# Kernel optimization log

Measured on AMD Instinct MI355X. Metric: run time of the kernel, lower is better.

## Reference

```python
import jax, jax.numpy as jnp
import numpy as np

C = 64  # channels fixed by module

def conv1x1(x, W, b):
    # x: [B,C,H,W], W: [C_out,C_in], b: [C_out]
    return jnp.einsum('bchw,oc->bohw', x, W) + b[None, :, None, None]

def setup_inputs() -> dict:
    key = jax.random.key(0)
    ks = jax.random.split(key, 16)
    B, H, W = 4, 64, 64
    inp = {
        'x_latter': jax.random.normal(ks[0], (B, C, H, W), jnp.float32),
        'x': jax.random.normal(ks[1], (B, C, H, W), jnp.float32),
    }
    scale = 1.0 / np.sqrt(C)
    names = ['high', 'low', 'value', 'e_conv', 'mid', 'latter']
    for i, n in enumerate(names):
        inp[f'W_{n}'] = jax.random.normal(ks[2 + 2 * i], (C, C), jnp.float32) * scale
        inp[f'b_{n}'] = jax.random.normal(ks[3 + 2 * i], (C,), jnp.float32) * 0.01
    return inp

def reference(x_latter, x, W_high, b_high, W_low, b_low, W_value, b_value,
              W_e_conv, b_e_conv, W_mid, b_mid, W_latter, b_latter):
    b, c, h, w = x_latter.shape
    hw = h * w
    # stage 1: channel-normalized spatial attention
    xl_hi = conv1x1(x_latter, W_high, b_high).reshape(b, c, hw)          # [b,c,hw]
    x_low = conv1x1(x, W_low, b_low).reshape(b, c, hw).transpose(0, 2, 1)  # [b,hw,c]
    p = jnp.einsum('bnc,bcm->bnm', x_low, xl_hi)                          # [b,hw,hw]
    p = jax.nn.softmax(p, axis=1)  # torch Softmax(dim=1) over first hw axis
    v = conv1x1(x, W_value, b_value).reshape(b, c, hw).transpose(0, 2, 1)  # [b,hw,c]
    e = jnp.einsum('bnm,bmc->bnc', p, v) + x_low                          # [b,hw,c]
    e = e.transpose(0, 2, 1).reshape(b, c, h, w)                          # [b,c,h,w]
    e = conv1x1(e, W_e_conv, b_e_conv).reshape(b, c, hw)                  # [b,c,hw]
    # stage 2: channel-channel attention
    xl2 = conv1x1(x_latter, W_latter, b_latter).reshape(b, c, hw).transpose(0, 2, 1)  # [b,hw,c]
    t = jnp.einsum('bcn,bnd->bcd', e, xl2)                                # [b,c,c]
    t = jax.nn.softmax(t, axis=1)
    x_mid = conv1x1(x, W_mid, b_mid).reshape(b, c, hw).transpose(0, 2, 1)  # [b,hw,c]
    out = jnp.einsum('bnc,bcd->bnd', x_mid, t)                            # [b,hw,c]
    return out.transpose(0, 2, 1).reshape(b, c, h, w)
```

## Files before the change

### kernel.cpp

```cpp
#include <hip/hip_runtime.h>
#include <math.h>

#define BATCH 4
#define CH 64
#define HW 4096

typedef __attribute__((ext_vector_type(8))) short short8;
typedef __attribute__((ext_vector_type(4))) float f32x4;
typedef __attribute__((ext_vector_type(4))) float float4v;

#define MFMA(a, b, c) __builtin_amdgcn_mfma_f32_16x16x32_bf16(a, b, c, 0, 0, 0)

__device__ __forceinline__ short f2bf(float f) {
    unsigned u = __builtin_bit_cast(unsigned, f);
    u += 0x7fffu + ((u >> 16) & 1u);
    return (short)(u >> 16);
}
__device__ __forceinline__ float bf2f(short s) {
    unsigned u = ((unsigned)(unsigned short)s) << 16;
    return __builtin_bit_cast(float, u);
}
__device__ __forceinline__ void gld16(const short* g, short* l) {
    __builtin_amdgcn_global_load_lds(
        (const __attribute__((address_space(1))) unsigned int*)g,
        (__attribute__((address_space(3))) unsigned int*)l, 16, 0, 0);
}

__global__ __launch_bounds__(256) void splitX(
    const float* __restrict__ x, const float* __restrict__ xl,
    short* __restrict__ XFh, short* __restrict__ XFl)
{
    int src = blockIdx.z, b = blockIdx.y, bx = blockIdx.x;
    const float* X = src ? xl : x;
    int t = threadIdx.x, wv = t >> 6, ln = t & 63;
    int nt = bx * 4 + wv;
    int n = (nt << 4) + (ln & 15);
    int g = ln >> 4;
    size_t sb = ((size_t)(src * BATCH + b) * 256 + nt) * 2;
    #pragma unroll
    for (int kt = 0; kt < 2; kt++) {
        short8 h, l;
        #pragma unroll
        for (int j = 0; j < 8; j++) {
            float v = X[(size_t)(b * 64 + kt * 32 + g * 8 + j) * HW + n];
            short hh = f2bf(v);
            h[j] = hh;
            l[j] = f2bf(v - bf2f(hh));
        }
        *(short8*)(XFh + (sb + kt) * 512 + (size_t)ln * 8) = h;
        *(short8*)(XFl + (sb + kt) * 512 + (size_t)ln * 8) = l;
    }
}

__global__ __launch_bounds__(256) void convm(
    const short* __restrict__ XFh, const short* __restrict__ XFl,
    const float* __restrict__ Wlow, const float* __restrict__ blow,
    const float* __restrict__ Wval, const float* __restrict__ bval,
    const float* __restrict__ Wmid, const float* __restrict__ bmid,
    const float* __restrict__ Wlat, const float* __restrict__ blat,
    const float* __restrict__ Whigh, const float* __restrict__ bhigh,
    float* __restrict__ XLOW, float* __restrict__ XMID, float* __restrict__ XL2,
    short* __restrict__ PAh, short* __restrict__ PAl,
    short* __restrict__ PBh, short* __restrict__ PBl,
    short* __restrict__ PVh, short* __restrict__ PVl)
{
    int mode = blockIdx.z, b = blockIdx.y, bx = blockIdx.x;
    const float* W; const float* bias; int src;
    switch (mode) {
        case 0:  W = Wlow;  bias = blow;  src = 0; break;
        case 1:  W = Wval;  bias = bval;  src = 0; break;
        case 2:  W = Wmid;  bias = bmid;  src = 0; break;
        case 3:  W = Wlat;  bias = blat;  src = 1; break;
        default: W = Whigh; bias = bhigh; src = 1; break;
    }
    int t = threadIdx.x, wv = t >> 6, ln = t & 63;
    int row = ln & 15, g = ln >> 4;

    short8 Wh[4][2], Wlo[4][2];
    #pragma unroll
    for (int ot = 0; ot < 4; ot++)
        #pragma unroll
        for (int kt = 0; kt < 2; kt++) {
            const float* wp = W + (ot * 16 + row) * 64 + kt * 32 + g * 8;
            short8 h, l;
            #pragma unroll
            for (int j = 0; j < 8; j++) {
                float v = wp[j];
                short hh = f2bf(v);
                h[j] = hh;
                l[j] = f2bf(v - bf2f(hh));
            }
            Wh[ot][kt] = h; Wlo[ot][kt] = l;
        }

    int nt = bx * 4 + wv;
    size_t xb = ((size_t)(src * BATCH + b) * 256 + nt) * 2;
    short8 Bh[2], Bl[2];
    #pragma unroll
    for (int kt = 0; kt < 2; kt++) {
        Bh[kt] = *(const short8*)(XFh + (xb + kt) * 512 + (size_t)ln * 8);
        Bl[kt] = *(const short8*)(XFl + (xb + kt) * 512 + (size_t)ln * 8);
    }

    f32x4 acc[4];
    #pragma unroll
    for (int ot = 0; ot < 4; ot++) {
        #pragma unroll
        for (int r = 0; r < 4; r++) acc[ot][r] = bias[ot * 16 + g * 4 + r];
    }
    #pragma unroll
    for (int ot = 0; ot < 4; ot++)
        #pragma unroll
        for (int kt = 0; kt < 2; kt++) {
            acc[ot] = MFMA(Wh[ot][kt], Bh[kt], acc[ot]);
            acc[ot] = MFMA(Wh[ot][kt], Bl[kt], acc[ot]);
            acc[ot] = MFMA(Wlo[ot][kt], Bh[kt], acc[ot]);
        }

    __shared__ float Ld[64][65];
    #pragma unroll
    for (int ot = 0; ot < 4; ot++)
        #pragma unroll
        for (int r = 0; r < 4; r++)
            Ld[wv * 16 + (ln & 15)][ot * 16 + g * 4 + r] = acc[ot][r];
    __syncthreads();

    int n0 = bx * 64;
    if (mode == 0 || mode == 2 || mode == 3) {
        float* outp = (mode == 0) ? XLOW : (mode == 2) ? XMID : XL2;
        int n = t >> 2, o0 = (t & 3) * 16;
        float vout[16];
        #pragma unroll
        for (int k = 0; k < 16; k++) vout[k] = Ld[n][o0 + k];
        float* gp = outp + ((size_t)b * HW + n0 + n) * 64 + o0;
        #pragma unroll
        for (int k = 0; k < 4; k++)
            *(float4v*)(gp + k * 4) = *(float4v*)(vout + k * 4);
    }
    if (mode == 0 || mode == 4) {
        short* Ph = (mode == 0) ? PAh : PBh;
        short* Pl = (mode == 0) ? PAl : PBl;
        #pragma unroll
        for (int kt = 0; kt < 2; kt++) {
            short8 h, l;
            #pragma unroll
            for (int j = 0; j < 8; j++) {
                float v = Ld[wv * 16 + (ln & 15)][kt * 32 + g * 8 + j];
                short hh = f2bf(v);
                h[j] = hh;
                l[j] = f2bf(v - bf2f(hh));
            }
            size_t blob = (((size_t)b * 256 + bx * 4 + wv) * 2 + kt) * 512 + (size_t)ln * 8;
            *(short8*)(Ph + blob) = h;
            *(short8*)(Pl + blob) = l;
        }
    }
    if (mode == 1) {
        int ktm_l = wv >> 1;
        int ct0 = (wv & 1) * 2;
        #pragma unroll
        for (int cc = 0; cc < 2; cc++) {
            int ct = ct0 + cc;
            int c = ct * 16 + (ln & 15);
            short8 h, l;
            #pragma unroll
            for (int j = 0; j < 8; j++) {
                float v = Ld[(ktm_l * 2 + (j >> 2)) * 16 + g * 4 + (j & 3)][c];
                short hh = f2bf(v);
                h[j] = hh;
                l[j] = f2bf(v - bf2f(hh));
            }
            size_t blob = (((size_t)b * 128 + bx * 2 + ktm_l) * 4 + ct) * 512 + (size_t)ln * 8;
            *(short8*)(PVh + blob) = h;
            *(short8*)(PVl + blob) = l;
        }
    }
}

__global__ __launch_bounds__(256) void zpass2(
    const short* __restrict__ PAh, const short* __restrict__ PAl,
    const short* __restrict__ PBh, const short* __restrict__ PBl,
    float* __restrict__ Zp)
{
    int bid = blockIdx.x;
    int sw = (bid & 7) * 128 + (bid >> 3);
    int mchunk = sw & 63, nc = (sw >> 6) & 3, b = sw >> 8;
    int t = threadIdx.x, wv = t >> 6, ln = t & 63;
    short8 bh[4][2], bl[4][2];
    #pragma unroll
    for (int msub = 0; msub < 4; msub++)
        #pragma unroll
        for (int kt = 0; kt < 2; kt++) {
            size_t o = ((size_t)(b * 256 + mchunk * 4 + msub) * 2 + kt) * 512 + ln * 8;
            bh[msub][kt] = *(const short8*)(PBh + o);
            bl[msub][kt] = *(const short8*)(PBl + o);
        }
    float zacc[4] = {0.f, 0.f, 0.f, 0.f};
    for (int s = 0; s < 16; s++) {
        int nt = nc * 64 + s * 4 + wv;
        size_t ab = ((size_t)(b * 256 + nt) * 2) * 512 + ln * 8;
        short8 ah0 = *(const short8*)(PAh + ab);
        short8 ah1 = *(const short8*)(PAh + ab + 512);
        short8 al0 = *(const short8*)(PAl + ab);
        short8 al1 = *(const short8*)(PAl + ab + 512);
        #pragma unroll
        for (int msub = 0; msub < 4; msub++) {
            f32x4 acc = {0.f, 0.f, 0.f, 0.f};
            acc = MFMA(ah0, bh[msub][0], acc);
            acc = MFMA(ah1, bh[msub][1], acc);
            acc = MFMA(ah0, bl[msub][0], acc);
            acc = MFMA(ah1, bl[msub][1], acc);
            acc = MFMA(al0, bh[msub][0], acc);
            acc = MFMA(al1, bh[msub][1], acc);
            zacc[msub] += __expf(acc[0]) + __expf(acc[1]) + __expf(acc[2]) + __expf(acc[3]);
        }
    }
    #pragma unroll
    for (int msub = 0; msub < 4; msub++) {
        zacc[msub] += __shfl_xor(zacc[msub], 16, 64);
        zacc[msub] += __shfl_xor(zacc[msub], 32, 64);
    }
    __shared__ float sZ[4][64];
    if (ln < 16) {
        #pragma unroll
        for (int msub = 0; msub < 4; msub++) sZ[wv][msub * 16 + ln] = zacc[msub];
    }
    __syncthreads();
    if (t < 64) {
        float z = sZ[0][t] + sZ[1][t] + sZ[2][t] + sZ[3][t];
        Zp[((size_t)(b * 4 + nc)) * 4096 + mchunk * 64 + t] = z;
    }
}

__global__ __launch_bounds__(256, 3) void epass8(
    const short* __restrict__ PAh, const short* __restrict__ PAl,
    const short* __restrict__ PBh, const short* __restrict__ PBl,
    const short* __restrict__ PVh, const short* __restrict__ PVl,
    const float* __restrict__ Zp, float* __restrict__ Ep, int nseg)
{
    int nwg = 32 * nseg * 4, cpx = nwg >> 3;
    int bid = blockIdx.x;
    int sw = (bid & 7) * cpx + (bid >> 3);
    int nb = sw & 31, mseg = (sw >> 5) % nseg, b = sw / (32 * nseg);
    int iters = 128 / nseg;
    int mper = 4096 / nseg;
    int t = threadIdx.x, wv = t >> 6, ln = t & 63;
    int lnm = ln & 15, lnr = ln >> 4;

    __shared__ __align__(16) short sB[2][2][2048];
    __shared__ __align__(16) short sV[2][2][2048];
    __shared__ __align__(16) float sZi[1024];

    for (int k = t; k < mper; k += 256) {
        int m = mseg * mper + k;
        float z = Zp[((size_t)(b * 4 + 0)) * 4096 + m]
                + Zp[((size_t)(b * 4 + 1)) * 4096 + m]
                + Zp[((size_t)(b * 4 + 2)) * 4096 + m]
                + Zp[((size_t)(b * 4 + 3)) * 4096 + m];
        sZi[k] = 1.f / z;
    }

    short8 Lh[2][2], Ll[2][2];
    #pragma unroll
    for (int rt = 0; rt < 2; rt++)
        #pragma unroll
        for (int kt = 0; kt < 2; kt++) {
            int nt = nb * 8 + wv * 2 + rt;
            size_t base = ((size_t)(b * 256 + nt) * 2 + kt) * 512 + ln * 8;
            Lh[rt][kt] = *(const short8*)(PAh + base);
            Ll[rt][kt] = *(const short8*)(PAl + base);
        }

    f32x4 acc_e[2][4];
    #pragma unroll
    for (int rt = 0; rt < 2; rt++)
        #pragma unroll
        for (int ct = 0; ct < 4; ct++) acc_e[rt][ct] = (f32x4){0.f, 0.f, 0.f, 0.f};

    const int mt00 = mseg * (mper >> 4);
    const int ktm0 = mseg * (mper >> 5);
    #define STAGE(bufi, ii) { \
        size_t pbb = (size_t)b * 262144 + (size_t)(mt00 + (ii) * 2) * 1024; \
        size_t pvb = (size_t)b * 262144 + (size_t)(ktm0 + (ii)) * 2048; \
        gld16(PBh + pbb + t * 8, &sB[bufi][0][wv * 512]); \
        gld16(PBl + pbb + t * 8, &sB[bufi][1][wv * 512]); \
        gld16(PVh + pvb + t * 8, &sV[bufi][0][wv * 512]); \
        gld16(PVl + pvb + t * 8, &sV[bufi][1][wv * 512]); }

    STAGE(0, 0);
    __syncthreads();

    for (int i = 0; i < iters; i++) {
        int cur = i & 1;
        if (i + 1 < iters) STAGE(cur ^ 1, i + 1);

        f32x4 wf[2][2];
        #pragma unroll
        for (int ms = 0; ms < 2; ms++) {
            const short8 bh0 = *(const short8*)&sB[cur][0][(ms * 2 + 0) * 512 + ln * 8];
            const short8 bh1 = *(const short8*)&sB[cur][0][(ms * 2 + 1) * 512 + ln * 8];
            const short8 bl0 = *(const short8*)&sB[cur][1][(ms * 2 + 0) * 512 + ln * 8];
            const short8 bl1 = *(const short8*)&sB[cur][1][(ms * 2 + 1) * 512 + ln * 8];
            const f32x4 vz = *(const f32x4*)&sZi[i * 32 + ms * 16 + lnr * 4];
            __builtin_amdgcn_s_setprio(1);
            #pragma unroll
            for (int rt = 0; rt < 2; rt++) {
                f32x4 acc = {0.f, 0.f, 0.f, 0.f};
                acc = MFMA(bh0, Lh[rt][0], acc);
                acc = MFMA(bh1, Lh[rt][1], acc);
                acc = MFMA(bh0, Ll[rt][0], acc);
                acc = MFMA(bh1, Ll[rt][1], acc);
                acc = MFMA(bl0, Lh[rt][0], acc);
                acc = MFMA(bl1, Lh[rt][1], acc);
                #pragma unroll
                for (int r = 0; r < 4; r++)
                    wf[rt][ms][r] = __expf(acc[r]) * vz[r];
            }
            __builtin_amdgcn_s_setprio(0);
        }
        short8 pah[2], pal[2];
        #pragma unroll
        for (int rt = 0; rt < 2; rt++) {
            short8 h, l;
            #pragma unroll
            for (int j = 0; j < 8; j++) {
                float w = wf[rt][j >> 2][j & 3];
                short hh = f2bf(w);
                h[j] = hh;
                l[j] = f2bf(w - bf2f(hh));
            }
            pah[rt] = h; pal[rt] = l;
        }
        __builtin_amdgcn_s_setprio(1);
        #pragma unroll
        for (int ct = 0; ct < 4; ct++) {
            const short8 vh = *(const short8*)&sV[cur][0][ct * 512 + ln * 8];
            const short8 vl = *(const short8*)&sV[cur][1][ct * 512 + ln * 8];
            #pragma unroll
            for (int rt = 0; rt < 2; rt++) {
                acc_e[rt][ct] = MFMA(pah[rt], vh, acc_e[rt][ct]);
                acc_e[rt][ct] = MFMA(pah[rt], vl, acc_e[rt][ct]);
                acc_e[rt][ct] = MFMA(pal[rt], vh, acc_e[rt][ct]);
            }
        }
        __builtin_amdgcn_s_setprio(0);
        __syncthreads();
    }
    #undef STAGE

    float* ep = Ep + ((size_t)mseg * BATCH + b) * HW * 64;
    #pragma unroll
    for (int rt = 0; rt < 2; rt++) {
        int n0 = (nb * 8 + wv * 2 + rt) * 16 + lnr * 4;
        #pragma unroll
        for (int ct = 0; ct < 4; ct++) {
            #pragma unroll
            for (int r = 0; r < 4; r++)
                ep[(size_t)(n0 + r) * 64 + ct * 16 + lnm] = acc_e[rt][ct][r];
        }
    }
}

template <int NSEG>
__global__ __launch_bounds__(256) void econv6(
    const float* __restrict__ Ep, const float* __restrict__ XLOW,
    const float* __restrict__ W, const float* __restrict__ bias,
    float* __restrict__ E2)
{
    const size_t SEG = (size_t)BATCH * HW * 64;
    int b = blockIdx.y, n0 = blockIdx.x * 64, t = threadIdx.x;
    __shared__ float Wl[64][64];
    __shared__ float El[64][65];
    for (int i = t; i < 4096; i += 256) Wl[i >> 6][i & 63] = W[i];
    for (int q = t; q < 1024; q += 256) {
        int nl = q >> 4, c0 = (q & 15) * 4;
        size_t idx = ((size_t)b * HW + n0 + nl) * 64 + c0;
        float4v s = *(const float4v*)(XLOW + idx);
        #pragma unroll
        for (int sg = 0; sg < NSEG; sg++) {
            float4v p = *(const float4v*)(Ep + sg * SEG + idx);
            s.x += p.x; s.y += p.y; s.z += p.z; s.w += p.w;
        }
        El[nl][c0] = s.x; El[nl][c0 + 1] = s.y;
        El[nl][c0 + 2] = s.z; El[nl][c0 + 3] = s.w;
    }
    __syncthreads();
    int nl = t & 63, og = t >> 6;
    for (int k = 0; k < 16; k++) {
        int o = og * 16 + k;
        float a0 = bias[o], a1 = 0.f, a2 = 0.f, a3 = 0.f;
        #pragma unroll
        for (int c = 0; c < 64; c += 4) {
            a0 += Wl[o][c]     * El[nl][c];
            a1 += Wl[o][c + 1] * El[nl][c + 1];
            a2 += Wl[o][c + 2] * El[nl][c + 2];
            a3 += Wl[o][c + 3] * El[nl][c + 3];
        }
        E2[((size_t)b * 64 + o) * HW + n0 + nl] = (a0 + a1) + (a2 + a3);
    }
}

__global__ __launch_bounds__(1024) void tmat(
    const float* __restrict__ E2, const float* __restrict__ XL2, float* __restrict__ T)
{
    int b = blockIdx.y, c = blockIdx.x, t = threadIdx.x;
    int d = t & 63, nl = t >> 6;
    const float* e = E2 + ((size_t)b * 64 + c) * HW;
    const float* x2 = XL2 + (size_t)b * HW * 64;
    float a0 = 0.f, a1 = 0.f;
    #pragma unroll 4
    for (int k = 0; k < 256; k += 2) {
        int na = k * 16 + nl, nb2 = na + 16;
        a0 += e[na] * x2[(size_t)na * 64 + d];
        a1 += e[nb2] * x2[(size_t)nb2 * 64 + d];
    }
    __shared__ float red[16][64];
    red[nl][d] = a0 + a1;
    __syncthreads();
    if (t < 64) {
        float s = 0.f;
        #pragma unroll
        for (int j = 0; j < 16; j++) s += red[j][t];
        T[((size_t)b * 64 + c) * 64 + t] = s;
    }
}

__global__ __launch_bounds__(64) void softT(
    const float* __restrict__ T, float* __restrict__ Ts)
{
    int d = blockIdx.x, b = blockIdx.y, c = threadIdx.x;
    float v = T[((size_t)b * 64 + c) * 64 + d];
    float M = v;
    #pragma unroll
    for (int o = 32; o > 0; o >>= 1) M = fmaxf(M, __shfl_xor(M, o, 64));
    float ez = __expf(v - M);
    float Z = ez;
    #pragma unroll
    for (int o = 32; o > 0; o >>= 1) Z += __shfl_xor(Z, o, 64);
    Ts[((size_t)b * 64 + c) * 64 + d] = ez / Z;
}

__global__ __launch_bounds__(256) void outk(
    const float* __restrict__ XMID, const float* __restrict__ Ts, float* __restrict__ out)
{
    int b = blockIdx.y, n0 = blockIdx.x * 64, t = threadIdx.x;
    __shared__ float Xm[64][65];
    __shared__ float Tl[64][64];
    for (int i = t; i < 4096; i += 256) {
        int nl = i >> 6, c = i & 63;
        Xm[nl][c] = XMID[((size_t)b * HW + n0 + nl) * 64 + c];
    }
    for (int i = t; i < 4096; i += 256) Tl[i >> 6][i & 63] = Ts[(size_t)b * 4096 + i];
    __syncthreads();
    int nl = t & 63, dg = t >> 6;
    float accs[16];
    #pragma unroll
    for (int k = 0; k < 16; k++) accs[k] = 0.f;
    for (int c = 0; c < 64; c++) {
        float xv = Xm[nl][c];
        #pragma unroll
        for (int k = 0; k < 16; k++) accs[k] += xv * Tl[c][dg * 16 + k];
    }
    #pragma unroll
    for (int k = 0; k < 16; k++) {
        int d = dg * 16 + k;
        out[((size_t)b * 64 + d) * HW + n0 + nl] = accs[k];
    }
}

extern "C" void kernel_launch(void* const* d_in, const int* in_sizes, int n_in,
                              void* d_out, int out_size, void* d_ws, size_t ws_size,
                              hipStream_t stream)
{
    const float* x_latter = (const float*)d_in[0];
    const float* x        = (const float*)d_in[1];
    const float* W_high = (const float*)d_in[2];  const float* b_high = (const float*)d_in[3];
    const float* W_low  = (const float*)d_in[4];  const float* b_low  = (const float*)d_in[5];
    const float* W_val  = (const float*)d_in[6];  const float* b_val  = (const float*)d_in[7];
    const float* W_ec   = (const float*)d_in[8];  const float* b_ec   = (const float*)d_in[9];
    const float* W_mid  = (const float*)d_in[10]; const float* b_mid  = (const float*)d_in[11];
    const float* W_lat  = (const float*)d_in[12]; const float* b_lat  = (const float*)d_in[13];
    float* outp = (float*)d_out;

    const size_t MAT = (size_t)BATCH * CH * HW;

    const size_t fixed_f = 3 * MAT + (size_t)BATCH * 4 * HW + 2 * (size_t)BATCH * 64 * 64;
    const size_t need8 = (fixed_f + 8 * MAT) * 4 + 6 * MAT * 2;
    int nseg = (ws_size >= need8) ? 8 : 4;

    float* ws = (float*)d_ws;
    size_t off = 0;
    float* XLOW = ws + off; off += MAT;
    float* XMID = ws + off; off += MAT;
    float* XL2  = ws + off; off += MAT;
    float* Zp   = ws + off; off += (size_t)BATCH * 4 * HW;
    float* T    = ws + off; off += (size_t)BATCH * 64 * 64;
    float* Ts   = ws + off; off += (size_t)BATCH * 64 * 64;
    short* sp = (short*)(ws + off);
    short* PAh = sp; sp += MAT;
    short* PAl = sp; sp += MAT;
    short* PBh = sp; sp += MAT;
    short* PBl = sp; sp += MAT;
    short* PVh = sp; sp += MAT;
    short* PVl = sp; sp += MAT;
    float* Ep  = (float*)sp;
    float* E2  = (float*)PAh;
    short* XFh = (short*)Ep;
    short* XFl = XFh + 2 * BATCH * 262144;

    splitX<<<dim3(64, BATCH, 2), 256, 0, stream>>>(x, x_latter, XFh, XFl);
    convm<<<dim3(64, BATCH, 5), 256, 0, stream>>>(
        XFh, XFl, W_low, b_low, W_val, b_val, W_mid, b_mid, W_lat, b_lat,
        W_high, b_high, XLOW, XMID, XL2, PAh, PAl, PBh, PBl, PVh, PVl);
    zpass2<<<dim3(1024), 256, 0, stream>>>(PAh, PAl, PBh, PBl, Zp);
    epass8<<<dim3(32 * nseg * 4), 256, 0, stream>>>(
        PAh, PAl, PBh, PBl, PVh, PVl, Zp, Ep, nseg);
    if (nseg == 8)
        econv6<8><<<dim3(64, BATCH), 256, 0, stream>>>(Ep, XLOW, W_ec, b_ec, E2);
    else
        econv6<4><<<dim3(64, BATCH), 256, 0, stream>>>(Ep, XLOW, W_ec, b_ec, E2);
    tmat<<<dim3(64, BATCH), 1024, 0, stream>>>(E2, XL2, T);
    softT<<<dim3(64, BATCH), 64, 0, stream>>>(T, Ts);
    outk<<<dim3(64, BATCH), 256, 0, stream>>>(XMID, Ts, outp);
}
```

Measured before the change: 150.3 us.

## Reassociate e_conv into channel-attention matrix and fuse softmax into output kernel

Instead of applying the e_conv 1x1 conv to the full [c,hw] tensor and then computing T, the code first accumulates M1 = E·XL2ᵀ and the column sums of XL2 with atomics. It then forms T = W·M1 + bias·sumᵀ inside the output kernel, together with the softmax, which removes the E2 round-trip and the tmat and softT launches. Separately, the bf16 hi/lo splitting now uses packed v_cvt_pk_bf16_f32 instructions in place of manual bit rounding. The trade-offs are float atomics, which make accumulation order nondeterministic, a memset launch, and a T that every outk2 block recomputes redundantly.

```diff
diff --git a/kernel.cpp b/kernel.cpp
--- a/kernel.cpp
+++ b/kernel.cpp
@@ -8,6 +8,7 @@
 typedef __attribute__((ext_vector_type(8))) short short8;
 typedef __attribute__((ext_vector_type(4))) float f32x4;
 typedef __attribute__((ext_vector_type(4))) float float4v;
+typedef __attribute__((ext_vector_type(4))) unsigned int uint4v;
 
 #define MFMA(a, b, c) __builtin_amdgcn_mfma_f32_16x16x32_bf16(a, b, c, 0, 0, 0)
 
@@ -19,6 +20,15 @@
 __device__ __forceinline__ float bf2f(short s) {
     unsigned u = ((unsigned)(unsigned short)s) << 16;
     return __builtin_bit_cast(float, u);
+}
+__device__ __forceinline__ void cvtpk2(float a, float b, unsigned &h, unsigned &l) {
+    unsigned hv;
+    asm("v_cvt_pk_bf16_f32 %0, %1, %2" : "=v"(hv) : "v"(a), "v"(b));
+    float ra = a - __builtin_bit_cast(float, hv << 16);
+    float rb = b - __builtin_bit_cast(float, hv & 0xffff0000u);
+    unsigned lv;
+    asm("v_cvt_pk_bf16_f32 %0, %1, %2" : "=v"(lv) : "v"(ra), "v"(rb));
+    h = hv; l = lv;
 }
 __device__ __forceinline__ void gld16(const short* g, short* l) {
     __builtin_amdgcn_global_load_lds(
@@ -39,16 +49,19 @@
     size_t sb = ((size_t)(src * BATCH + b) * 256 + nt) * 2;
     #pragma unroll
     for (int kt = 0; kt < 2; kt++) {
-        short8 h, l;
-        #pragma unroll
-        for (int j = 0; j < 8; j++) {
-            float v = X[(size_t)(b * 64 + kt * 32 + g * 8 + j) * HW + n];
-            short hh = f2bf(v);
-            h[j] = hh;
-            l[j] = f2bf(v - bf2f(hh));
-        }
-        *(short8*)(XFh + (sb + kt) * 512 + (size_t)ln * 8) = h;
-        *(short8*)(XFl + (sb + kt) * 512 + (size_t)ln * 8) = l;
+        float v[8];
+        #pragma unroll
+        for (int j = 0; j < 8; j++)
+            v[j] = X[(size_t)(b * 64 + kt * 32 + g * 8 + j) * HW + n];
+        uint4v hw, lw;
+        #pragma unroll
+        for (int k2 = 0; k2 < 4; k2++) {
+            unsigned h, l;
+            cvtpk2(v[2 * k2], v[2 * k2 + 1], h, l);
+            hw[k2] = h; lw[k2] = l;
+        }
+        *(uint4v*)(XFh + (sb + kt) * 512 + (size_t)ln * 8) = hw;
+        *(uint4v*)(XFl + (sb + kt) * 512 + (size_t)ln * 8) = lw;
     }
 }
 
@@ -82,15 +95,15 @@
         #pragma unroll
         for (int kt = 0; kt < 2; kt++) {
             const float* wp = W + (ot * 16 + row) * 64 + kt * 32 + g * 8;
-            short8 h, l;
-            #pragma unroll
-            for (int j = 0; j < 8; j++) {
-                float v = wp[j];
-                short hh = f2bf(v);
-                h[j] = hh;
-                l[j] = f2bf(v - bf2f(hh));
-            }
-            Wh[ot][kt] = h; Wlo[ot][kt] = l;
+            uint4v hw, lw;
+            #pragma unroll
+            for (int k2 = 0; k2 < 4; k2++) {
+                unsigned h, l;
+                cvtpk2(wp[2 * k2], wp[2 * k2 + 1], h, l);
+                hw[k2] = h; lw[k2] = l;
+            }
+            Wh[ot][kt] = __builtin_bit_cast(short8, hw);
+            Wlo[ot][kt] = __builtin_bit_cast(short8, lw);
         }
 
     int nt = bx * 4 + wv;
@@ -142,17 +155,17 @@
         short* Pl = (mode == 0) ? PAl : PBl;
         #pragma unroll
         for (int kt = 0; kt < 2; kt++) {
-            short8 h, l;
-            #pragma unroll
-            for (int j = 0; j < 8; j++) {
-                float v = Ld[wv * 16 + (ln & 15)][kt * 32 + g * 8 + j];
-                short hh = f2bf(v);
-                h[j] = hh;
-                l[j] = f2bf(v - bf2f(hh));
+            uint4v hw, lw;
+            #pragma unroll
+            for (int k2 = 0; k2 < 4; k2++) {
+                unsigned h, l;
+                cvtpk2(Ld[wv * 16 + (ln & 15)][kt * 32 + g * 8 + 2 * k2],
+                       Ld[wv * 16 + (ln & 15)][kt * 32 + g * 8 + 2 * k2 + 1], h, l);
+                hw[k2] = h; lw[k2] = l;
             }
             size_t blob = (((size_t)b * 256 + bx * 4 + wv) * 2 + kt) * 512 + (size_t)ln * 8;
-            *(short8*)(Ph + blob) = h;
-            *(short8*)(Pl + blob) = l;
+            *(uint4v*)(Ph + blob) = hw;
+            *(uint4v*)(Pl + blob) = lw;
         }
     }
     if (mode == 1) {
@@ -162,17 +175,20 @@
         for (int cc = 0; cc < 2; cc++) {
             int ct = ct0 + cc;
             int c = ct * 16 + (ln & 15);
-            short8 h, l;
-            #pragma unroll
-            for (int j = 0; j < 8; j++) {
-                float v = Ld[(ktm_l * 2 + (j >> 2)) * 16 + g * 4 + (j & 3)][c];
-                short hh = f2bf(v);
-                h[j] = hh;
-                l[j] = f2bf(v - bf2f(hh));
+            float v[8];
+            #pragma unroll
+            for (int j = 0; j < 8; j++)
+                v[j] = Ld[(ktm_l * 2 + (j >> 2)) * 16 + g * 4 + (j & 3)][c];
+            uint4v hw, lw;
+            #pragma unroll
+            for (int k2 = 0; k2 < 4; k2++) {
+                unsigned h, l;
+                cvtpk2(v[2 * k2], v[2 * k2 + 1], h, l);
+                hw[k2] = h; lw[k2] = l;
             }
             size_t blob = (((size_t)b * 128 + bx * 2 + ktm_l) * 4 + ct) * 512 + (size_t)ln * 8;
-            *(short8*)(PVh + blob) = h;
-            *(short8*)(PVl + blob) = l;
+            *(uint4v*)(PVh + blob) = hw;
+            *(uint4v*)(PVl + blob) = lw;
         }
     }
 }
@@ -232,7 +248,7 @@
     }
 }
 
-__global__ __launch_bounds__(256, 3) void epass8(
+__global__ __launch_bounds__(256, 3) void epass9(
     const short* __restrict__ PAh, const short* __restrict__ PAl,
     const short* __restrict__ PBh, const short* __restrict__ PBl,
     const short* __restrict__ PVh, const short* __restrict__ PVl,
@@ -321,15 +337,16 @@
         short8 pah[2], pal[2];
         #pragma unroll
         for (int rt = 0; rt < 2; rt++) {
-            short8 h, l;
-            #pragma unroll
-            for (int j = 0; j < 8; j++) {
-                float w = wf[rt][j >> 2][j & 3];
-                short hh = f2bf(w);
-                h[j] = hh;
-                l[j] = f2bf(w - bf2f(hh));
-            }
-            pah[rt] = h; pal[rt] = l;
+            uint4v hw, lw;
+            #pragma unroll
+            for (int k2 = 0; k2 < 4; k2++) {
+                unsigned h, l;
+                cvtpk2(wf[rt][k2 >> 1][2 * (k2 & 1)],
+                       wf[rt][k2 >> 1][2 * (k2 & 1) + 1], h, l);
+                hw[k2] = h; lw[k2] = l;
+            }
+            pah[rt] = __builtin_bit_cast(short8, hw);
+            pal[rt] = __builtin_bit_cast(short8, lw);
         }
         __builtin_amdgcn_s_setprio(1);
         #pragma unroll
@@ -362,108 +379,138 @@
 }
 
 template <int NSEG>
-__global__ __launch_bounds__(256) void econv6(
+__global__ __launch_bounds__(256) void emat(
     const float* __restrict__ Ep, const float* __restrict__ XLOW,
+    const float* __restrict__ XL2, float* __restrict__ M1s)
+{
+    const size_t SEG = (size_t)BATCH * HW * 64;
+    int b = blockIdx.y, t = threadIdx.x;
+    __shared__ float El[64][65];
+    __shared__ float X2[64][68];
+    int c = t & 63, dg = t >> 6;
+    float acc[16];
+    #pragma unroll
+    for (int k = 0; k < 16; k++) acc[k] = 0.f;
+    float ssum = 0.f;
+
+    for (int half = 0; half < 2; half++) {
+        int n0 = (blockIdx.x * 2 + half) * 64;
+        __syncthreads();
+        for (int q = t; q < 1024; q += 256) {
+            int nl = q >> 4, c0 = (q & 15) * 4;
+            size_t idx = ((size_t)b * HW + n0 + nl) * 64 + c0;
+            float4v sv = *(const float4v*)(XLOW + idx);
+            #pragma unroll
+            for (int sg = 0; sg < NSEG; sg++) {
+                float4v p = *(const float4v*)(Ep + sg * SEG + idx);
+                sv.x += p.x; sv.y += p.y; sv.z += p.z; sv.w += p.w;
+            }
+            El[nl][c0] = sv.x; El[nl][c0 + 1] = sv.y;
+            El[nl][c0 + 2] = sv.z; El[nl][c0 + 3] = sv.w;
+            float4v xv = *(const float4v*)(XL2 + idx);
+            X2[nl][c0] = xv.x; X2[nl][c0 + 1] = xv.y;
+            X2[nl][c0 + 2] = xv.z; X2[nl][c0 + 3] = xv.w;
+        }
+        __syncthreads();
+        for (int nl = 0; nl < 64; nl++) {
+            float e = El[nl][c];
+            const float4v xa = *(const float4v*)&X2[nl][dg * 16];
+            const float4v xb = *(const float4v*)&X2[nl][dg * 16 + 4];
+            const float4v xc = *(const float4v*)&X2[nl][dg * 16 + 8];
+            const float4v xd = *(const float4v*)&X2[nl][dg * 16 + 12];
+            acc[0] += e * xa.x; acc[1] += e * xa.y; acc[2] += e * xa.z; acc[3] += e * xa.w;
+            acc[4] += e * xb.x; acc[5] += e * xb.y; acc[6] += e * xb.z; acc[7] += e * xb.w;
+            acc[8] += e * xc.x; acc[9] += e * xc.y; acc[10] += e * xc.z; acc[11] += e * xc.w;
+            acc[12] += e * xd.x; acc[13] += e * xd.y; acc[14] += e * xd.z; acc[15] += e * xd.w;
+        }
+        if (t < 64) {
+            float s2 = 0.f;
+            #pragma unroll 8
+            for (int nl = 0; nl < 64; nl++) s2 += X2[nl][t];
+            ssum += s2;
+        }
+    }
+    float* M1 = M1s;
+    float* svec = M1s + BATCH * 64 * 64;
+    #pragma unroll
+    for (int k = 0; k < 16; k++)
+        atomicAdd(&M1[((size_t)b * 64 + c) * 64 + dg * 16 + k], acc[k]);
+    if (t < 64) atomicAdd(&svec[b * 64 + t], ssum);
+}
+
+__global__ __launch_bounds__(256) void outk2(
+    const float* __restrict__ XMID, const float* __restrict__ M1s,
     const float* __restrict__ W, const float* __restrict__ bias,
-    float* __restrict__ E2)
-{
-    const size_t SEG = (size_t)BATCH * HW * 64;
+    float* __restrict__ out)
+{
     int b = blockIdx.y, n0 = blockIdx.x * 64, t = threadIdx.x;
-    __shared__ float Wl[64][64];
-    __shared__ float El[64][65];
+    const float* M1 = M1s;
+    const float* svec = M1s + BATCH * 64 * 64;
+    __shared__ float Wl[64][65];
+    __shared__ float Ml[64][68];
+    __shared__ float Pl[64][65];
+    __shared__ float Xm[64][65];
+    __shared__ float Md[64], Zd[64];
+
     for (int i = t; i < 4096; i += 256) Wl[i >> 6][i & 63] = W[i];
     for (int q = t; q < 1024; q += 256) {
-        int nl = q >> 4, c0 = (q & 15) * 4;
-        size_t idx = ((size_t)b * HW + n0 + nl) * 64 + c0;
-        float4v s = *(const float4v*)(XLOW + idx);
-        #pragma unroll
-        for (int sg = 0; sg < NSEG; sg++) {
-            float4v p = *(const float4v*)(Ep + sg * SEG + idx);
-            s.x += p.x; s.y += p.y; s.z += p.z; s.w += p.w;
-        }
-        El[nl][c0] = s.x; El[nl][c0 + 1] = s.y;
-        El[nl][c0 + 2] = s.z; El[nl][c0 + 3] = s.w;
-    }
-    __syncthreads();
-    int nl = t & 63, og = t >> 6;
-    for (int k = 0; k < 16; k++) {
-        int o = og * 16 + k;
-        float a0 = bias[o], a1 = 0.f, a2 = 0.f, a3 = 0.f;
-        #pragma unroll
-        for (int c = 0; c < 64; c += 4) {
-            a0 += Wl[o][c]     * El[nl][c];
-            a1 += Wl[o][c + 1] * El[nl][c + 1];
-            a2 += Wl[o][c + 2] * El[nl][c + 2];
-            a3 += Wl[o][c + 3] * El[nl][c + 3];
-        }
-        E2[((size_t)b * 64 + o) * HW + n0 + nl] = (a0 + a1) + (a2 + a3);
-    }
-}
-
-__global__ __launch_bounds__(1024) void tmat(
-    const float* __restrict__ E2, const float* __restrict__ XL2, float* __restrict__ T)
-{
-    int b = blockIdx.y, c = blockIdx.x, t = threadIdx.x;
-    int d = t & 63, nl = t >> 6;
-    const float* e = E2 + ((size_t)b * 64 + c) * HW;
-    const float* x2 = XL2 + (size_t)b * HW * 64;
-    float a0 = 0.f, a1 = 0.f;
-    #pragma unroll 4
-    for (int k = 0; k < 256; k += 2) {
-        int na = k * 16 + nl, nb2 = na + 16;
-        a0 += e[na] * x2[(size_t)na * 64 + d];
-        a1 += e[nb2] * x2[(size_t)nb2 * 64 + d];
-    }
-    __shared__ float red[16][64];
-    red[nl][d] = a0 + a1;
-    __syncthreads();
-    if (t < 64) {
-        float s = 0.f;
-        #pragma unroll
-        for (int j = 0; j < 16; j++) s += red[j][t];
-        T[((size_t)b * 64 + c) * 64 + t] = s;
-    }
-}
-
-__global__ __launch_bounds__(64) void softT(
-    const float* __restrict__ T, float* __restrict__ Ts)
-{
-    int d = blockIdx.x, b = blockIdx.y, c = threadIdx.x;
-    float v = T[((size_t)b * 64 + c) * 64 + d];
-    float M = v;
-    #pragma unroll
-    for (int o = 32; o > 0; o >>= 1) M = fmaxf(M, __shfl_xor(M, o, 64));
-    float ez = __expf(v - M);
-    float Z = ez;
-    #pragma unroll
-    for (int o = 32; o > 0; o >>= 1) Z += __shfl_xor(Z, o, 64);
-    Ts[((size_t)b * 64 + c) * 64 + d] = ez / Z;
-}
-
-__global__ __launch_bounds__(256) void outk(
-    const float* __restrict__ XMID, const float* __restrict__ Ts, float* __restrict__ out)
-{
-    int b = blockIdx.y, n0 = blockIdx.x * 64, t = threadIdx.x;
-    __shared__ float Xm[64][65];
-    __shared__ float Tl[64][64];
+        int cc = q >> 4, d0 = (q & 15) * 4;
+        float4v m4 = *(const float4v*)(M1 + ((size_t)b * 64 + cc) * 64 + d0);
+        Ml[cc][d0] = m4.x; Ml[cc][d0 + 1] = m4.y;
+        Ml[cc][d0 + 2] = m4.z; Ml[cc][d0 + 3] = m4.w;
+    }
     for (int i = t; i < 4096; i += 256) {
         int nl = i >> 6, c = i & 63;
         Xm[nl][c] = XMID[((size_t)b * HW + n0 + nl) * 64 + c];
     }
-    for (int i = t; i < 4096; i += 256) Tl[i >> 6][i & 63] = Ts[(size_t)b * 4096 + i];
-    __syncthreads();
-    int nl = t & 63, dg = t >> 6;
+    __syncthreads();
+
+    int cp = t & 63, dg = t >> 6;
+    {
+        float bi = bias[cp];
+        float tacc[16];
+        #pragma unroll
+        for (int k = 0; k < 16; k++) tacc[k] = bi * svec[b * 64 + dg * 16 + k];
+        for (int cc = 0; cc < 64; cc++) {
+            float w = Wl[cp][cc];
+            const float4v ma = *(const float4v*)&Ml[cc][dg * 16];
+            const float4v mb = *(const float4v*)&Ml[cc][dg * 16 + 4];
+            const float4v mc = *(const float4v*)&Ml[cc][dg * 16 + 8];
+            const float4v md = *(const float4v*)&Ml[cc][dg * 16 + 12];
+            tacc[0] += w * ma.x; tacc[1] += w * ma.y; tacc[2] += w * ma.z; tacc[3] += w * ma.w;
+            tacc[4] += w * mb.x; tacc[5] += w * mb.y; tacc[6] += w * mb.z; tacc[7] += w * mb.w;
+            tacc[8] += w * mc.x; tacc[9] += w * mc.y; tacc[10] += w * mc.z; tacc[11] += w * mc.w;
+            tacc[12] += w * md.x; tacc[13] += w * md.y; tacc[14] += w * md.z; tacc[15] += w * md.w;
+        }
+        #pragma unroll
+        for (int k = 0; k < 16; k++) Pl[cp][dg * 16 + k] = tacc[k];
+    }
+    __syncthreads();
+    if (t < 64) {
+        float M = Pl[0][t];
+        for (int c = 1; c < 64; c++) M = fmaxf(M, Pl[c][t]);
+        float Z = 0.f;
+        for (int c = 0; c < 64; c++) Z += __expf(Pl[c][t] - M);
+        Md[t] = M; Zd[t] = 1.f / Z;
+    }
+    __syncthreads();
+    for (int i = t; i < 4096; i += 256) {
+        int c = i >> 6, d = i & 63;
+        Pl[c][d] = __expf(Pl[c][d] - Md[d]) * Zd[d];
+    }
+    __syncthreads();
+    int nl = t & 63, dg2 = t >> 6;
     float accs[16];
     #pragma unroll
     for (int k = 0; k < 16; k++) accs[k] = 0.f;
     for (int c = 0; c < 64; c++) {
         float xv = Xm[nl][c];
         #pragma unroll
-        for (int k = 0; k < 16; k++) accs[k] += xv * Tl[c][dg * 16 + k];
+        for (int k = 0; k < 16; k++) accs[k] += xv * Pl[c][dg2 * 16 + k];
     }
     #pragma unroll
     for (int k = 0; k < 16; k++) {
-        int d = dg * 16 + k;
+        int d = dg2 * 16 + k;
         out[((size_t)b * 64 + d) * HW + n0 + nl] = accs[k];
     }
 }
@@ -483,8 +530,9 @@
     float* outp = (float*)d_out;
 
     const size_t MAT = (size_t)BATCH * CH * HW;
-
-    const size_t fixed_f = 3 * MAT + (size_t)BATCH * 4 * HW + 2 * (size_t)BATCH * 64 * 64;
+    const size_t M1N = (size_t)BATCH * 64 * 64 + BATCH * 64;
+
+    const size_t fixed_f = 3 * MAT + (size_t)BATCH * 4 * HW + M1N;
     const size_t need8 = (fixed_f + 8 * MAT) * 4 + 6 * MAT * 2;
     int nseg = (ws_size >= need8) ? 8 : 4;
 
@@ -494,8 +542,7 @@
     float* XMID = ws + off; off += MAT;
     float* XL2  = ws + off; off += MAT;
     float* Zp   = ws + off; off += (size_t)BATCH * 4 * HW;
-    float* T    = ws + off; off += (size_t)BATCH * 64 * 64;
-    float* Ts   = ws + off; off += (size_t)BATCH * 64 * 64;
+    float* M1s  = ws + off; off += M1N;
     short* sp = (short*)(ws + off);
     short* PAh = sp; sp += MAT;
     short* PAl = sp; sp += MAT;
@@ -504,22 +551,20 @@
     short* PVh = sp; sp += MAT;
     short* PVl = sp; sp += MAT;
     float* Ep  = (float*)sp;
-    float* E2  = (float*)PAh;
     short* XFh = (short*)Ep;
     short* XFl = XFh + 2 * BATCH * 262144;
 
+    hipMemsetAsync(M1s, 0, M1N * sizeof(float), stream);
     splitX<<<dim3(64, BATCH, 2), 256, 0, stream>>>(x, x_latter, XFh, XFl);
     convm<<<dim3(64, BATCH, 5), 256, 0, stream>>>(
         XFh, XFl, W_low, b_low, W_val, b_val, W_mid, b_mid, W_lat, b_lat,
         W_high, b_high, XLOW, XMID, XL2, PAh, PAl, PBh, PBl, PVh, PVl);
     zpass2<<<dim3(1024), 256, 0, stream>>>(PAh, PAl, PBh, PBl, Zp);
-    epass8<<<dim3(32 * nseg * 4), 256, 0, stream>>>(
+    epass9<<<dim3(32 * nseg * 4), 256, 0, stream>>>(
         PAh, PAl, PBh, PBl, PVh, PVl, Zp, Ep, nseg);
     if (nseg == 8)
-        econv6<8><<<dim3(64, BATCH), 256, 0, stream>>>(Ep, XLOW, W_ec, b_ec, E2);
+        emat<8><<<dim3(32, BATCH), 256, 0, stream>>>(Ep, XLOW, XL2, M1s);
     else
-        econv6<4><<<dim3(64, BATCH), 256, 0, stream>>>(Ep, XLOW, W_ec, b_ec, E2);
-    tmat<<<dim3(64, BATCH), 1024, 0, stream>>>(E2, XL2, T);
-    softT<<<dim3(64, BATCH), 64, 0, stream>>>(T, Ts);
-    outk<<<dim3(64, BATCH), 256, 0, stream>>>(XMID, Ts, outp);
-}
+        emat<4><<<dim3(32, BATCH), 256, 0, stream>>>(Ep, XLOW, XL2, M1s);
+    outk2<<<dim3(64, BATCH), 256, 0, stream>>>(XMID, M1s, W_ec, b_ec, outp);
+}
```

Measured after the change: 155.9 us. 3.8% more time.

## Fuse input bf16 split into convm, use packed bf16 converts and exp2

Applied to the files above, without the earlier changes.

Removes the separate splitX kernel: convm now reads fp32 x and x_latter directly and splits them into bf16 hi/lo pairs in registers. All software bf16 rounding loops are replaced by the packed v_cvt_pk_bf16_f32 instruction, two values at a time. The high-projection operand is pre-scaled by log2(e) so the softmax exponentials in zpass2 and epass can use the native exp2 instead of __expf. In exchange convm performs five-fold redundant strided fp32 loads of x and the conversion work per mode, and the pre-scaling slightly changes rounding of the hi/lo split.

```diff
diff --git a/kernel.cpp b/kernel.cpp
--- a/kernel.cpp
+++ b/kernel.cpp
@@ -4,21 +4,30 @@
 #define BATCH 4
 #define CH 64
 #define HW 4096
+#define LOG2E 1.4426950408889634f
 
 typedef __attribute__((ext_vector_type(8))) short short8;
 typedef __attribute__((ext_vector_type(4))) float f32x4;
 typedef __attribute__((ext_vector_type(4))) float float4v;
+typedef __attribute__((ext_vector_type(4))) unsigned int uint4v;
 
 #define MFMA(a, b, c) __builtin_amdgcn_mfma_f32_16x16x32_bf16(a, b, c, 0, 0, 0)
 
-__device__ __forceinline__ short f2bf(float f) {
-    unsigned u = __builtin_bit_cast(unsigned, f);
-    u += 0x7fffu + ((u >> 16) & 1u);
-    return (short)(u >> 16);
-}
-__device__ __forceinline__ float bf2f(short s) {
-    unsigned u = ((unsigned)(unsigned short)s) << 16;
-    return __builtin_bit_cast(float, u);
+__device__ __forceinline__ float exp2v(float x) {
+#if __has_builtin(__builtin_amdgcn_exp2f)
+    return __builtin_amdgcn_exp2f(x);
+#else
+    return exp2f(x);
+#endif
+}
+__device__ __forceinline__ void cvtpk2(float a, float b, unsigned &h, unsigned &l) {
+    unsigned hv;
+    asm("v_cvt_pk_bf16_f32 %0, %1, %2" : "=v"(hv) : "v"(a), "v"(b));
+    float ra = a - __builtin_bit_cast(float, hv << 16);
+    float rb = b - __builtin_bit_cast(float, hv & 0xffff0000u);
+    unsigned lv;
+    asm("v_cvt_pk_bf16_f32 %0, %1, %2" : "=v"(lv) : "v"(ra), "v"(rb));
+    h = hv; l = lv;
 }
 __device__ __forceinline__ void gld16(const short* g, short* l) {
     __builtin_amdgcn_global_load_lds(
@@ -26,34 +35,8 @@
         (__attribute__((address_space(3))) unsigned int*)l, 16, 0, 0);
 }
 
-__global__ __launch_bounds__(256) void splitX(
+__global__ __launch_bounds__(256) void convm(
     const float* __restrict__ x, const float* __restrict__ xl,
-    short* __restrict__ XFh, short* __restrict__ XFl)
-{
-    int src = blockIdx.z, b = blockIdx.y, bx = blockIdx.x;
-    const float* X = src ? xl : x;
-    int t = threadIdx.x, wv = t >> 6, ln = t & 63;
-    int nt = bx * 4 + wv;
-    int n = (nt << 4) + (ln & 15);
-    int g = ln >> 4;
-    size_t sb = ((size_t)(src * BATCH + b) * 256 + nt) * 2;
-    #pragma unroll
-    for (int kt = 0; kt < 2; kt++) {
-        short8 h, l;
-        #pragma unroll
-        for (int j = 0; j < 8; j++) {
-            float v = X[(size_t)(b * 64 + kt * 32 + g * 8 + j) * HW + n];
-            short hh = f2bf(v);
-            h[j] = hh;
-            l[j] = f2bf(v - bf2f(hh));
-        }
-        *(short8*)(XFh + (sb + kt) * 512 + (size_t)ln * 8) = h;
-        *(short8*)(XFl + (sb + kt) * 512 + (size_t)ln * 8) = l;
-    }
-}
-
-__global__ __launch_bounds__(256) void convm(
-    const short* __restrict__ XFh, const short* __restrict__ XFl,
     const float* __restrict__ Wlow, const float* __restrict__ blow,
     const float* __restrict__ Wval, const float* __restrict__ bval,
     const float* __restrict__ Wmid, const float* __restrict__ bmid,
@@ -65,13 +48,13 @@
     short* __restrict__ PVh, short* __restrict__ PVl)
 {
     int mode = blockIdx.z, b = blockIdx.y, bx = blockIdx.x;
-    const float* W; const float* bias; int src;
+    const float* W; const float* bias; const float* X;
     switch (mode) {
-        case 0:  W = Wlow;  bias = blow;  src = 0; break;
-        case 1:  W = Wval;  bias = bval;  src = 0; break;
-        case 2:  W = Wmid;  bias = bmid;  src = 0; break;
-        case 3:  W = Wlat;  bias = blat;  src = 1; break;
-        default: W = Whigh; bias = bhigh; src = 1; break;
+        case 0:  W = Wlow;  bias = blow;  X = x;  break;
+        case 1:  W = Wval;  bias = bval;  X = x;  break;
+        case 2:  W = Wmid;  bias = bmid;  X = x;  break;
+        case 3:  W = Wlat;  bias = blat;  X = xl; break;
+        default: W = Whigh; bias = bhigh; X = xl; break;
     }
     int t = threadIdx.x, wv = t >> 6, ln = t & 63;
     int row = ln & 15, g = ln >> 4;
@@ -82,24 +65,34 @@
         #pragma unroll
         for (int kt = 0; kt < 2; kt++) {
             const float* wp = W + (ot * 16 + row) * 64 + kt * 32 + g * 8;
-            short8 h, l;
-            #pragma unroll
-            for (int j = 0; j < 8; j++) {
-                float v = wp[j];
-                short hh = f2bf(v);
-                h[j] = hh;
-                l[j] = f2bf(v - bf2f(hh));
+            uint4v hw, lw;
+            #pragma unroll
+            for (int k2 = 0; k2 < 4; k2++) {
+                unsigned h, l;
+                cvtpk2(wp[2 * k2], wp[2 * k2 + 1], h, l);
+                hw[k2] = h; lw[k2] = l;
             }
-            Wh[ot][kt] = h; Wlo[ot][kt] = l;
+            Wh[ot][kt] = __builtin_bit_cast(short8, hw);
+            Wlo[ot][kt] = __builtin_bit_cast(short8, lw);
         }
 
     int nt = bx * 4 + wv;
-    size_t xb = ((size_t)(src * BATCH + b) * 256 + nt) * 2;
     short8 Bh[2], Bl[2];
     #pragma unroll
     for (int kt = 0; kt < 2; kt++) {
-        Bh[kt] = *(const short8*)(XFh + (xb + kt) * 512 + (size_t)ln * 8);
-        Bl[kt] = *(const short8*)(XFl + (xb + kt) * 512 + (size_t)ln * 8);
+        float v[8];
+        #pragma unroll
+        for (int j = 0; j < 8; j++)
+            v[j] = X[(size_t)(b * 64 + kt * 32 + g * 8 + j) * HW + nt * 16 + row];
+        uint4v hw, lw;
+        #pragma unroll
+        for (int k2 = 0; k2 < 4; k2++) {
+            unsigned h, l;
+            cvtpk2(v[2 * k2], v[2 * k2 + 1], h, l);
+            hw[k2] = h; lw[k2] = l;
+        }
+        Bh[kt] = __builtin_bit_cast(short8, hw);
+        Bl[kt] = __builtin_bit_cast(short8, lw);
     }
 
     f32x4 acc[4];
@@ -140,19 +133,20 @@
     if (mode == 0 || mode == 4) {
         short* Ph = (mode == 0) ? PAh : PBh;
         short* Pl = (mode == 0) ? PAl : PBl;
+        float scale = (mode == 4) ? LOG2E : 1.0f;
         #pragma unroll
         for (int kt = 0; kt < 2; kt++) {
-            short8 h, l;
-            #pragma unroll
-            for (int j = 0; j < 8; j++) {
-                float v = Ld[wv * 16 + (ln & 15)][kt * 32 + g * 8 + j];
-                short hh = f2bf(v);
-                h[j] = hh;
-                l[j] = f2bf(v - bf2f(hh));
+            uint4v hw, lw;
+            #pragma unroll
+            for (int k2 = 0; k2 < 4; k2++) {
+                unsigned h, l;
+                cvtpk2(Ld[wv * 16 + (ln & 15)][kt * 32 + g * 8 + 2 * k2] * scale,
+                       Ld[wv * 16 + (ln & 15)][kt * 32 + g * 8 + 2 * k2 + 1] * scale, h, l);
+                hw[k2] = h; lw[k2] = l;
             }
             size_t blob = (((size_t)b * 256 + bx * 4 + wv) * 2 + kt) * 512 + (size_t)ln * 8;
-            *(short8*)(Ph + blob) = h;
-            *(short8*)(Pl + blob) = l;
+            *(uint4v*)(Ph + blob) = hw;
+            *(uint4v*)(Pl + blob) = lw;
         }
     }
     if (mode == 1) {
@@ -162,17 +156,20 @@
         for (int cc = 0; cc < 2; cc++) {
             int ct = ct0 + cc;
             int c = ct * 16 + (ln & 15);
-            short8 h, l;
-            #pragma unroll
-            for (int j = 0; j < 8; j++) {
-                float v = Ld[(ktm_l * 2 + (j >> 2)) * 16 + g * 4 + (j & 3)][c];
-                short hh = f2bf(v);
-                h[j] = hh;
-                l[j] = f2bf(v - bf2f(hh));
+            float v[8];
+            #pragma unroll
+            for (int j = 0; j < 8; j++)
+                v[j] = Ld[(ktm_l * 2 + (j >> 2)) * 16 + g * 4 + (j & 3)][c];
+            uint4v hw, lw;
+            #pragma unroll
+            for (int k2 = 0; k2 < 4; k2++) {
+                unsigned h, l;
+                cvtpk2(v[2 * k2], v[2 * k2 + 1], h, l);
+                hw[k2] = h; lw[k2] = l;
             }
             size_t blob = (((size_t)b * 128 + bx * 2 + ktm_l) * 4 + ct) * 512 + (size_t)ln * 8;
-            *(short8*)(PVh + blob) = h;
-            *(short8*)(PVl + blob) = l;
+            *(uint4v*)(PVh + blob) = hw;
+            *(uint4v*)(PVl + blob) = lw;
         }
     }
 }
@@ -212,7 +209,7 @@
             acc = MFMA(ah1, bl[msub][1], acc);
             acc = MFMA(al0, bh[msub][0], acc);
             acc = MFMA(al1, bh[msub][1], acc);
-            zacc[msub] += __expf(acc[0]) + __expf(acc[1]) + __expf(acc[2]) + __expf(acc[3]);
+            zacc[msub] += exp2v(acc[0]) + exp2v(acc[1]) + exp2v(acc[2]) + exp2v(acc[3]);
         }
     }
     #pragma unroll
@@ -232,7 +229,7 @@
     }
 }
 
-__global__ __launch_bounds__(256, 3) void epass8(
+__global__ __launch_bounds__(256, 3) void epass10(
     const short* __restrict__ PAh, const short* __restrict__ PAl,
     const short* __restrict__ PBh, const short* __restrict__ PBl,
     const short* __restrict__ PVh, const short* __restrict__ PVl,
@@ -314,22 +311,23 @@
                 acc = MFMA(bl1, Lh[rt][1], acc);
                 #pragma unroll
                 for (int r = 0; r < 4; r++)
-                    wf[rt][ms][r] = __expf(acc[r]) * vz[r];
+                    wf[rt][ms][r] = exp2v(acc[r]) * vz[r];
             }
             __builtin_amdgcn_s_setprio(0);
         }
         short8 pah[2], pal[2];
         #pragma unroll
         for (int rt = 0; rt < 2; rt++) {
-            short8 h, l;
-            #pragma unroll
-            for (int j = 0; j < 8; j++) {
-                float w = wf[rt][j >> 2][j & 3];
-                short hh = f2bf(w);
-                h[j] = hh;
-                l[j] = f2bf(w - bf2f(hh));
+            uint4v hw, lw;
+            #pragma unroll
+            for (int k2 = 0; k2 < 4; k2++) {
+                unsigned h, l;
+                cvtpk2(wf[rt][k2 >> 1][2 * (k2 & 1)],
+                       wf[rt][k2 >> 1][2 * (k2 & 1) + 1], h, l);
+                hw[k2] = h; lw[k2] = l;
             }
-            pah[rt] = h; pal[rt] = l;
+            pah[rt] = __builtin_bit_cast(short8, hw);
+            pal[rt] = __builtin_bit_cast(short8, lw);
         }
         __builtin_amdgcn_s_setprio(1);
         #pragma unroll
@@ -505,15 +503,12 @@
     short* PVl = sp; sp += MAT;
     float* Ep  = (float*)sp;
     float* E2  = (float*)PAh;
-    short* XFh = (short*)Ep;
-    short* XFl = XFh + 2 * BATCH * 262144;
-
-    splitX<<<dim3(64, BATCH, 2), 256, 0, stream>>>(x, x_latter, XFh, XFl);
+
     convm<<<dim3(64, BATCH, 5), 256, 0, stream>>>(
-        XFh, XFl, W_low, b_low, W_val, b_val, W_mid, b_mid, W_lat, b_lat,
+        x, x_latter, W_low, b_low, W_val, b_val, W_mid, b_mid, W_lat, b_lat,
         W_high, b_high, XLOW, XMID, XL2, PAh, PAl, PBh, PBl, PVh, PVl);
     zpass2<<<dim3(1024), 256, 0, stream>>>(PAh, PAl, PBh, PBl, Zp);
-    epass8<<<dim3(32 * nseg * 4), 256, 0, stream>>>(
+    epass10<<<dim3(32 * nseg * 4), 256, 0, stream>>>(
         PAh, PAl, PBh, PBl, PVh, PVl, Zp, Ep, nseg);
     if (nseg == 8)
         econv6<8><<<dim3(64, BATCH), 256, 0, stream>>>(Ep, XLOW, W_ec, b_ec, E2);
```

New measurement: 139.5 us, median of 2. 1.08x faster.
